# Kernel tuning notes

Measured on AMD Instinct MI355X. Metric: run time of the kernel, lower is better.

Reference implementation:

```python
import math
import jax, jax.numpy as jnp
import numpy as np

MAX_RADIUS = 10.0
N_BASIS = 10   # number_of_basis
H = 100        # radial MLP hidden width
EPS = 1e-6


def _radial(r, w1, w2, w3):
    """CosineBasisModel: cosine-bump radial basis followed by a swish MLP.
    r: [B,N,N] pair distances -> [B,N,N,C*C] per-pair kernel weights."""
    radii = jnp.linspace(0.0, MAX_RADIUS, N_BASIS)
    step = radii[1] - radii[0]
    u = (r[..., None] - radii) / step * (jnp.pi / 2)            # [B,N,N,R]
    basis = jnp.where(jnp.abs(u) < jnp.pi / 2, jnp.cos(u) ** 2, 0.0)
    h1 = jax.nn.silu(basis @ w1 * (1.0 / math.sqrt(N_BASIS)))  # swish, fan-in norm (e3nn FC)
    h2 = jax.nn.silu(h1 @ w2 * (1.0 / math.sqrt(H)))
    return h2 @ w3 * (1.0 / math.sqrt(H))                       # [B,N,N,C*C]


def setup_inputs() -> dict:
    key = jax.random.key(0)
    ks = jax.random.split(key, 10)
    B, N1, N2, C = 8, 32, 32, 64
    return {
        "input1": jax.random.normal(ks[0], (B, N1, C), jnp.float32),
        "input2": jax.random.normal(ks[1], (B, N2, C), jnp.float32),
        "xyz1": jax.random.normal(ks[2], (B, N1, 3), jnp.float32) * 3.0,
        "xyz2": jax.random.normal(ks[3], (B, N2, 3), jnp.float32) * 3.0,
        "mask": jnp.ones((B, N1 + N2), jnp.int32),
        "w1": jax.random.normal(ks[4], (N_BASIS, H), jnp.float32),
        "w2": jax.random.normal(ks[5], (H, H), jnp.float32),
        "w3": jax.random.normal(ks[6], (H, C * C), jnp.float32),
        "fc3_w": jax.random.normal(ks[7], (C, C), jnp.float32),
        "fc2_w": jax.random.normal(ks[8], (C, 1), jnp.float32),
    }


def reference(input1, input2, xyz1, xyz2, mask, w1, w2, w3, fc3_w, fc2_w):
    x = jnp.concatenate((input1, input2), axis=1)        # [B,N,C]
    xyz = jnp.concatenate((xyz1, xyz2), axis=1)          # [B,N,3]
    B, N, C = x.shape
    # continuous-filter convolution: per-pair radial kernel, all-pairs scatter-sum
    diff = xyz[:, :, None, :] - xyz[:, None, :, :]       # [B,N,N,3]
    r = jnp.sqrt(jnp.sum(diff * diff, axis=-1) + 1e-12)  # [B,N,N]
    K = _radial(r, w1, w2, w3).reshape(B, N, N, C, C)    # [B,N,N,Cout,Cin]
    x = jnp.einsum('zaboi,zbi->zao', K, x) * (1.0 / math.sqrt(N))
    # Norm over irreps: for l=0 scalar irreps the norm is |x|
    x = jnp.abs(x)
    x = jnp.where(mask[:, :, None] != 0, x, 0.0)
    x = jnp.sum(x, axis=1)                               # [B,C]
    mean = x.mean(-1, keepdims=True)
    std = jnp.std(x, axis=-1, ddof=1, keepdims=True)     # torch.std is unbiased
    x = (x - mean) / (std + EPS)
    x = jax.nn.leaky_relu(x @ fc3_w * (1.0 / math.sqrt(C)))
    x = x @ fc2_w * (1.0 / math.sqrt(C))
    return jax.nn.sigmoid(x).reshape(-1)                 # [B]
```

## Files before the change

### kernel.cpp

```cpp
#include <hip/hip_runtime.h>
#include <math.h>

#define NB 10
#define HH 100
#define TABN 2048
#define TAB_MAX 11.2f
#define INV_DELTA ((float)TABN / TAB_MAX)


__global__ __launch_bounds__(256) void tm_kernel(
    const float* __restrict__ in1, const float* __restrict__ in2,
    const float* __restrict__ w1, const float* __restrict__ w2,
    const float* __restrict__ w3,
    float* __restrict__ tab, float* __restrict__ Mout)
{
    __shared__ float s_w1[NB * HH];
    __shared__ float s_basis[8][NB];
    __shared__ float s_h1[8][HH];
    __shared__ float s_x[16][64];

    int tid = threadIdx.x;

    if (blockIdx.x < 257) {
        for (int i = tid; i < NB * HH; i += 256) s_w1[i] = w1[i];

        int p0 = blockIdx.x * 8;
        const float DELTA = TAB_MAX / (float)TABN;
        const float STEP = 10.0f / 9.0f;
        const float HALF_PI = 1.57079632679489662f;

        if (tid < 8 * NB) {
            int p = tid / NB, j = tid % NB;
            float r = (float)(p0 + p) * DELTA;
            float u = (r - (float)j * STEP) * (HALF_PI / STEP);
            float c = __cosf(u);
            s_basis[p][j] = (fabsf(u) < HALF_PI) ? c * c : 0.0f;
        }
        __syncthreads();

        const float inv_sqrt10 = 0.31622776601683794f;
        for (int task = tid; task < 8 * HH; task += 256) {
            int p = task / HH, k = task % HH;
            float acc = 0.f;
            #pragma unroll
            for (int j = 0; j < NB; ++j) acc += s_basis[p][j] * s_w1[j * HH + k];
            acc *= inv_sqrt10;
            float sg = 1.0f / (1.0f + __expf(-acc));
            s_h1[p][k] = acc * sg;
        }
        __syncthreads();

        if (tid < 8 * 25) {
            int p = tid / 25, k2g = tid % 25;
            int idx = p0 + p;
            float4 acc = make_float4(0.f, 0.f, 0.f, 0.f);
            #pragma unroll 4
            for (int k = 0; k < HH; ++k) {
                float hv = s_h1[p][k];
                float4 wv = *(const float4*)(w2 + (size_t)k * HH + k2g * 4);
                acc.x += hv * wv.x; acc.y += hv * wv.y; acc.z += hv * wv.z; acc.w += hv * wv.w;
            }
            if (idx <= TABN) {
                float4 o; float a;
                a = acc.x * 0.1f; o.x = a / (1.0f + __expf(-a));
                a = acc.y * 0.1f; o.y = a / (1.0f + __expf(-a));
                a = acc.z * 0.1f; o.z = a / (1.0f + __expf(-a));
                a = acc.w * 0.1f; o.w = a / (1.0f + __expf(-a));
                *(float4*)(tab + (size_t)idx * HH + k2g * 4) = o;
            }
        }
    } else {
        int m = blockIdx.x - 257;
        int zbg = m / 7, yc = m % 7;

        {
            int lz = tid >> 4, q = tid & 15;
            int zb = zbg * 16 + lz;
            int z = zb >> 6, b = zb & 63;
            const float* src = (b < 32) ? (in1 + (size_t)(z * 32 + b) * 64)
                                        : (in2 + (size_t)(z * 32 + (b - 32)) * 64);
            *(float4*)&s_x[lz][q * 4] = *(const float4*)(src + q * 4);
        }
        __syncthreads();

        int task = yc * 256 + tid;
        if (task < 1600) {
            int h = task >> 4, og = task & 15;
            const float* wbase = w3 + (size_t)h * 4096 + og * 256;

            float4 acc[16];
            #pragma unroll
            for (int l = 0; l < 16; ++l) acc[l] = make_float4(0.f, 0.f, 0.f, 0.f);

            const float4* sx4 = (const float4*)s_x;
            #pragma unroll 2
            for (int i4 = 0; i4 < 16; ++i4) {
                float4 wa = *(const float4*)(wbase + i4 * 4);
                float4 wb = *(const float4*)(wbase + 64 + i4 * 4);
                float4 wc = *(const float4*)(wbase + 128 + i4 * 4);
                float4 wd = *(const float4*)(wbase + 192 + i4 * 4);
                #pragma unroll
                for (int l = 0; l < 16; ++l) {
                    float4 xv = sx4[l * 16 + i4];
                    acc[l].x += wa.x * xv.x + wa.y * xv.y + wa.z * xv.z + wa.w * xv.w;
                    acc[l].y += wb.x * xv.x + wb.y * xv.y + wb.z * xv.z + wb.w * xv.w;
                    acc[l].z += wc.x * xv.x + wc.y * xv.y + wc.z * xv.z + wc.w * xv.w;
                    acc[l].w += wd.x * xv.x + wd.y * xv.y + wd.z * xv.z + wd.w * xv.w;
                }
            }
            #pragma unroll
            for (int l = 0; l < 16; ++l) {
                int zb = zbg * 16 + l;
                *(float4*)(Mout + (size_t)zb * 6400 + h * 64 + og * 4) = acc[l];
            }
        }
    }
}

__global__ __launch_bounds__(256) void kernel_Y(
    const float* __restrict__ xyz1, const float* __restrict__ xyz2,
    const float* __restrict__ tab, const float* __restrict__ M,
    float* __restrict__ partial)
{
    __shared__ float s_M[6400];
    __shared__ float s_h2T[6400];
    __shared__ int   s_i0[64];
    __shared__ float s_f[64];

    const int z = blockIdx.x, b = blockIdx.y;
    const int tid = threadIdx.x;

    if (tid < 64) {
        int a = tid;
        const float* pa = (a < 32) ? (xyz1 + (size_t)(z * 32 + a) * 3)
                                   : (xyz2 + (size_t)(z * 32 + (a - 32)) * 3);
        const float* pb = (b < 32) ? (xyz1 + (size_t)(z * 32 + b) * 3)
                                   : (xyz2 + (size_t)(z * 32 + (b - 32)) * 3);
        float dx = pa[0] - pb[0], dy = pa[1] - pb[1], dz = pa[2] - pb[2];
        float r = sqrtf(dx * dx + dy * dy + dz * dz + 1e-12f);
        float t = r * INV_DELTA;
        int i0 = (int)t;
        i0 = (i0 < TABN - 1) ? i0 : (TABN - 1);
        float f = t - (float)i0;
        s_i0[a] = i0;
        s_f[a] = (f < 1.0f) ? f : 1.0f;
    }
    {
        const float4* Msrc = (const float4*)(M + (size_t)(z * 64 + b) * 6400);
        float4* sM4 = (float4*)s_M;
        for (int i = tid; i < 1600; i += 256) sM4[i] = Msrc[i];
    }
    __syncthreads();

    for (int task = tid; task < 1600; task += 256) {
        int a4 = task / 100, c = task - a4 * 100;
        float4 hv;
        #pragma unroll
        for (int k = 0; k < 4; ++k) {
            int a = a4 * 4 + k;
            int i0 = s_i0[a];
            float f = s_f[a];
            const float* tp = tab + (size_t)i0 * HH + c;
            float v0 = tp[0], v1 = tp[HH];
            ((float*)&hv)[k] = fmaf(f, v1 - v0, v0);
        }
        *(float4*)&s_h2T[c * 64 + ((a4 ^ (c & 7)) << 2)] = hv;
    }
    __syncthreads();

    const int og = tid & 15, ag = tid >> 4;
    float4 acc0 = make_float4(0.f, 0.f, 0.f, 0.f);
    float4 acc1 = make_float4(0.f, 0.f, 0.f, 0.f);
    float4 acc2 = make_float4(0.f, 0.f, 0.f, 0.f);
    float4 acc3 = make_float4(0.f, 0.f, 0.f, 0.f);

    #pragma unroll 4
    for (int c = 0; c < 100; ++c) {
        float4 mv = *(const float4*)&s_M[c * 64 + og * 4];
        float4 hv = *(const float4*)&s_h2T[c * 64 + ((ag ^ (c & 7)) << 2)];
        acc0.x += hv.x * mv.x; acc0.y += hv.x * mv.y; acc0.z += hv.x * mv.z; acc0.w += hv.x * mv.w;
        acc1.x += hv.y * mv.x; acc1.y += hv.y * mv.y; acc1.z += hv.y * mv.z; acc1.w += hv.y * mv.w;
        acc2.x += hv.z * mv.x; acc2.y += hv.z * mv.y; acc2.z += hv.z * mv.z; acc2.w += hv.z * mv.w;
        acc3.x += hv.w * mv.x; acc3.y += hv.w * mv.y; acc3.z += hv.w * mv.z; acc3.w += hv.w * mv.w;
    }

    size_t base = ((size_t)(z * 64 + b) * 64 + ag * 4) * 64 + og * 4;
    *(float4*)&partial[base]       = acc0;
    *(float4*)&partial[base + 64]  = acc1;
    *(float4*)&partial[base + 128] = acc2;
    *(float4*)&partial[base + 192] = acc3;
}

__global__ __launch_bounds__(1024) void kernel_rf(
    const float* __restrict__ partial, const int* __restrict__ mask,
    const float* __restrict__ fc3w, const float* __restrict__ fc2w,
    float* __restrict__ out)
{
    __shared__ float sred[16][64];
    __shared__ float s_sn[64];

    const int z = blockIdx.x;
    const int tid = threadIdx.x;
    const int o = tid & 63;
    const int aq = tid >> 6;

    float s0 = 0.f, s1 = 0.f, s2v = 0.f, s3 = 0.f;
    const float* pz = partial + (size_t)z * 262144 + (size_t)aq * 256 + o;
    #pragma unroll 4
    for (int b = 0; b < 64; ++b) {
        const float* p = pz + (size_t)b * 4096;
        s0 += p[0];
        s1 += p[64];
        s2v += p[128];
        s3 += p[192];
    }

    const float scale = 0.0125f;
    const int* mz = mask + z * 64 + aq * 4;
    float local = 0.f;
    local += (mz[0] != 0) ? fabsf(s0) * scale : 0.f;
    local += (mz[1] != 0) ? fabsf(s1) * scale : 0.f;
    local += (mz[2] != 0) ? fabsf(s2v) * scale : 0.f;
    local += (mz[3] != 0) ? fabsf(s3) * scale : 0.f;
    sred[aq][o] = local;
    __syncthreads();

    if (tid < 64) {
        float s = 0.f;
        #pragma unroll
        for (int g = 0; g < 16; ++g) s += sred[g][o];

        float tot = s;
        #pragma unroll
        for (int d = 32; d >= 1; d >>= 1) tot += __shfl_xor(tot, d, 64);
        float mean = tot * (1.0f / 64.0f);
        float dv = s - mean;
        float v2 = dv * dv;
        #pragma unroll
        for (int d = 32; d >= 1; d >>= 1) v2 += __shfl_xor(v2, d, 64);
        float var = v2 * (1.0f / 63.0f);
        s_sn[o] = dv / (sqrtf(var) + 1e-6f);
    }
    __syncthreads();

    if (tid < 64) {
        float accf = 0.f;
        #pragma unroll 8
        for (int i = 0; i < 64; ++i) accf += s_sn[i] * fc3w[i * 64 + o];
        accf *= 0.125f;
        float t = (accf > 0.f) ? accf : 0.01f * accf;
        float pr = t * fc2w[o];
        #pragma unroll
        for (int d = 32; d >= 1; d >>= 1) pr += __shfl_xor(pr, d, 64);
        if (o == 0 && tid < 64) out[z] = 1.0f / (1.0f + expf(-0.125f * pr));
    }
}

extern "C" void kernel_launch(void* const* d_in, const int* in_sizes, int n_in,
                              void* d_out, int out_size, void* d_ws, size_t ws_size,
                              hipStream_t stream) {
    const float* in1  = (const float*)d_in[0];
    const float* in2  = (const float*)d_in[1];
    const float* xyz1 = (const float*)d_in[2];
    const float* xyz2 = (const float*)d_in[3];
    const int*   mask = (const int*)d_in[4];
    const float* w1   = (const float*)d_in[5];
    const float* w2   = (const float*)d_in[6];
    const float* w3   = (const float*)d_in[7];
    const float* fc3w = (const float*)d_in[8];
    const float* fc2w = (const float*)d_in[9];
    float* out = (float*)d_out;

    float* ws      = (float*)d_ws;
    float* tab     = ws;
    float* Mg      = ws + 204900;
    float* partial = ws + 3481700;

    tm_kernel<<<481, 256, 0, stream>>>(in1, in2, w1, w2, w3, tab, Mg);
    kernel_Y<<<dim3(8, 64), 256, 0, stream>>>(xyz1, xyz2, tab, Mg, partial);
    kernel_rf<<<8, 1024, 0, stream>>>(partial, mask, fc3w, fc2w, out);
}
```

Baseline: 62.51 us.

## Fuse final reduction into kernel_Y via atomics and last-block tail

Removes the separate reduction kernel and the large partial buffer. Each kernel_Y block now atomically adds its 64x64 contribution into a small per-batch accumulator, and the last block per batch (found with an atomic counter) runs the norm, standardisation and MLP head. The accumulator and counter are zeroed inside tm_kernel. This saves one launch and about 8 MB of partial writes and reads, at the cost of 4096 float atomics per block contending on 8 batch slices and a reduction order that is no longer deterministic.

```diff
diff --git a/kernel.cpp b/kernel.cpp
--- a/kernel.cpp
+++ b/kernel.cpp
@@ -12,7 +12,8 @@
     const float* __restrict__ in1, const float* __restrict__ in2,
     const float* __restrict__ w1, const float* __restrict__ w2,
     const float* __restrict__ w3,
-    float* __restrict__ tab, float* __restrict__ Mout)
+    float* __restrict__ tab, float* __restrict__ Mout,
+    float* __restrict__ y, unsigned int* __restrict__ cnt)
 {
     __shared__ float s_w1[NB * HH];
     __shared__ float s_basis[8][NB];
@@ -20,6 +21,9 @@
     __shared__ float s_x[16][64];
 
     int tid = threadIdx.x;
+
+    if (blockIdx.x < 128) y[blockIdx.x * 256 + tid] = 0.f;
+    if (blockIdx.x == 0 && tid < 8) cnt[tid] = 0u;
 
     if (blockIdx.x < 257) {
         for (int i = tid; i < NB * HH; i += 256) s_w1[i] = w1[i];
@@ -120,12 +124,18 @@
 __global__ __launch_bounds__(256) void kernel_Y(
     const float* __restrict__ xyz1, const float* __restrict__ xyz2,
     const float* __restrict__ tab, const float* __restrict__ M,
-    float* __restrict__ partial)
+    float* __restrict__ y, unsigned int* __restrict__ cnt,
+    const int* __restrict__ mask,
+    const float* __restrict__ fc3w, const float* __restrict__ fc2w,
+    float* __restrict__ out)
 {
     __shared__ float s_M[6400];
     __shared__ float s_h2T[6400];
     __shared__ int   s_i0[64];
     __shared__ float s_f[64];
+    __shared__ float sred[4][64];
+    __shared__ float s_sn[64];
+    __shared__ unsigned int s_old;
 
     const int z = blockIdx.x, b = blockIdx.y;
     const int tid = threadIdx.x;
@@ -184,51 +194,43 @@
         acc3.x += hv.w * mv.x; acc3.y += hv.w * mv.y; acc3.z += hv.w * mv.z; acc3.w += hv.w * mv.w;
     }
 
-    size_t base = ((size_t)(z * 64 + b) * 64 + ag * 4) * 64 + og * 4;
-    *(float4*)&partial[base]       = acc0;
-    *(float4*)&partial[base + 64]  = acc1;
-    *(float4*)&partial[base + 128] = acc2;
-    *(float4*)&partial[base + 192] = acc3;
-}
-
-__global__ __launch_bounds__(1024) void kernel_rf(
-    const float* __restrict__ partial, const int* __restrict__ mask,
-    const float* __restrict__ fc3w, const float* __restrict__ fc2w,
-    float* __restrict__ out)
-{
-    __shared__ float sred[16][64];
-    __shared__ float s_sn[64];
-
-    const int z = blockIdx.x;
-    const int tid = threadIdx.x;
-    const int o = tid & 63;
-    const int aq = tid >> 6;
-
-    float s0 = 0.f, s1 = 0.f, s2v = 0.f, s3 = 0.f;
-    const float* pz = partial + (size_t)z * 262144 + (size_t)aq * 256 + o;
-    #pragma unroll 4
-    for (int b = 0; b < 64; ++b) {
-        const float* p = pz + (size_t)b * 4096;
-        s0 += p[0];
-        s1 += p[64];
-        s2v += p[128];
-        s3 += p[192];
-    }
-
-    const float scale = 0.0125f;
-    const int* mz = mask + z * 64 + aq * 4;
-    float local = 0.f;
-    local += (mz[0] != 0) ? fabsf(s0) * scale : 0.f;
-    local += (mz[1] != 0) ? fabsf(s1) * scale : 0.f;
-    local += (mz[2] != 0) ? fabsf(s2v) * scale : 0.f;
-    local += (mz[3] != 0) ? fabsf(s3) * scale : 0.f;
-    sred[aq][o] = local;
+    {
+        float* yz = y + (size_t)z * 4096 + (size_t)(ag * 4) * 64 + og * 4;
+        #pragma unroll
+        for (int j = 0; j < 4; ++j) {
+            atomicAdd(&yz[0 * 64 + j], ((float*)&acc0)[j]);
+            atomicAdd(&yz[1 * 64 + j], ((float*)&acc1)[j]);
+            atomicAdd(&yz[2 * 64 + j], ((float*)&acc2)[j]);
+            atomicAdd(&yz[3 * 64 + j], ((float*)&acc3)[j]);
+        }
+    }
+
+    __syncthreads();
+    if (tid == 0) {
+        s_old = __hip_atomic_fetch_add(&cnt[z], 1u, __ATOMIC_ACQ_REL,
+                                       __HIP_MEMORY_SCOPE_AGENT);
+    }
+    __syncthreads();
+    if (s_old != 63u) return;
+
+    __threadfence();
+    {
+        const int o = tid & 63, aq = tid >> 6;
+        const float scale = 0.0125f;
+        float local = 0.f;
+        #pragma unroll 4
+        for (int k = 0; k < 16; ++k) {
+            int a = aq * 16 + k;
+            float v = y[(size_t)z * 4096 + (size_t)a * 64 + o];
+            local += (mask[z * 64 + a] != 0) ? fabsf(v) * scale : 0.f;
+        }
+        sred[aq][o] = local;
+    }
     __syncthreads();
 
     if (tid < 64) {
-        float s = 0.f;
-        #pragma unroll
-        for (int g = 0; g < 16; ++g) s += sred[g][o];
+        int o = tid;
+        float s = sred[0][o] + sred[1][o] + sred[2][o] + sred[3][o];
 
         float tot = s;
         #pragma unroll
@@ -244,6 +246,7 @@
     __syncthreads();
 
     if (tid < 64) {
+        int o = tid;
         float accf = 0.f;
         #pragma unroll 8
         for (int i = 0; i < 64; ++i) accf += s_sn[i] * fc3w[i * 64 + o];
@@ -252,7 +255,7 @@
         float pr = t * fc2w[o];
         #pragma unroll
         for (int d = 32; d >= 1; d >>= 1) pr += __shfl_xor(pr, d, 64);
-        if (o == 0 && tid < 64) out[z] = 1.0f / (1.0f + expf(-0.125f * pr));
+        if (o == 0) out[z] = 1.0f / (1.0f + expf(-0.125f * pr));
     }
 }
 
@@ -271,12 +274,13 @@
     const float* fc2w = (const float*)d_in[9];
     float* out = (float*)d_out;
 
-    float* ws      = (float*)d_ws;
-    float* tab     = ws;
-    float* Mg      = ws + 204900;
-    float* partial = ws + 3481700;
-
-    tm_kernel<<<481, 256, 0, stream>>>(in1, in2, w1, w2, w3, tab, Mg);
-    kernel_Y<<<dim3(8, 64), 256, 0, stream>>>(xyz1, xyz2, tab, Mg, partial);
-    kernel_rf<<<8, 1024, 0, stream>>>(partial, mask, fc3w, fc2w, out);
+    float* ws   = (float*)d_ws;
+    float* tab  = ws;
+    float* Mg   = ws + 204900;
+    float* y    = ws + 3481700;
+    unsigned int* cnt = (unsigned int*)(ws + 3514468);
+
+    tm_kernel<<<481, 256, 0, stream>>>(in1, in2, w1, w2, w3, tab, Mg, y, cnt);
+    kernel_Y<<<dim3(8, 64), 256, 0, stream>>>(xyz1, xyz2, tab, Mg, y, cnt,
+                                              mask, fc3w, fc2w, out);
 }
```

After: 95.53 us. +52.8%, slower.
